# Optimization experiments

Hardware: AMD Instinct MI355X
Metric: run time of the kernel (lower is better)

The kernel has to match this reference:

```python
import jax, jax.numpy as jnp
import numpy as np
from jax import lax

B, N, C, RED = 8, 2048, 1024, 4
GN_EPS = 1e-5


def setup_inputs() -> dict:
    key = jax.random.key(0)
    ks = jax.random.split(key, 8)
    s = lambda k, shp, sc: jax.random.normal(k, shp, jnp.float32) * sc
    return dict(
        x=jax.random.normal(ks[0], (B, N, C), jnp.float32),
        qkv_w=s(ks[1], (C, 3 * C), 0.02),
        c1=jnp.float32(0.01 ** 2),
        c2=jnp.float32(0.03 ** 2),
        conv1_w=s(ks[2], (4, 1, 3), 0.3),      # OIH
        gn_g=jnp.ones(4, jnp.float32),
        gn_b=jnp.zeros(4, jnp.float32),
        conv2_w=s(ks[3], (1, 4, 3), 0.3),      # OIH
        conv2_b=jnp.zeros(1, jnp.float32),
        ch_w1=s(ks[4], (C, C // RED), 0.02),
        ch_b1=jnp.zeros(C // RED, jnp.float32),
        ch_w2=s(ks[5], (C // RED, C), 0.02),
        ch_b2=jnp.zeros(C, jnp.float32),
        proj_w=s(ks[6], (C, C), 0.02),
        proj_b=jnp.zeros(C, jnp.float32),
    )


def _conv1d(x, w):  # x:[B,Cin,N], w:[O,I,3], pad=1
    return lax.conv_general_dilated(x, w, (1,), [(1, 1)],
                                    dimension_numbers=('NCH', 'OIH', 'NCH'))


def _ode_func(A, conv1_w, gn_g, gn_b, conv2_w, conv2_b):
    # A: [B,N] -> Conv1d(1,4) -> GroupNorm(2,4) -> ReLU -> Conv1d(4,1)
    h = _conv1d(A[:, None, :], conv1_w)                 # [B,4,N]
    b, _, n = h.shape
    hg = h.reshape(b, 2, 2, n)                          # 2 groups of 2 channels
    mu = hg.mean((2, 3), keepdims=True)
    var = hg.var((2, 3), keepdims=True)
    h = ((hg - mu) * lax.rsqrt(var + GN_EPS)).reshape(b, 4, n)
    h = jax.nn.relu(h * gn_g[None, :, None] + gn_b[None, :, None])
    y = _conv1d(h, conv2_w) + conv2_b[None, :, None]    # [B,1,N]
    return y[:, 0, :]


def reference(x, qkv_w, c1, c2, conv1_w, gn_g, gn_b, conv2_w, conv2_b,
              ch_w1, ch_b1, ch_w2, ch_b2, proj_w, proj_b):
    Bx, Nx, Cx = x.shape
    qkv = (x @ qkv_w).reshape(Bx, Nx, 3, Cx)
    q, k, v = qkv[..., 0, :], qkv[..., 1, :], qkv[..., 2, :]

    # SSIM-style per-token statistics over the channel dim
    mu_q = q.mean(-1, keepdims=True)
    mu_k = k.mean(-1, keepdims=True)
    dq, dk = q - mu_q, k - mu_k
    inv_cm1 = 1.0 / (Cx - 1)
    sigma_qk = (dq * dk).sum(-1, keepdims=True) * inv_cm1
    sigma_q2 = (dq * dq).sum(-1, keepdims=True) * inv_cm1
    sigma_k2 = (dk * dk).sum(-1, keepdims=True) * inv_cm1
    num = (2 * mu_q * mu_k + c1) * (2 * sigma_qk + c2)
    den = (mu_q ** 2 + mu_k ** 2 + c1) * (sigma_q2 + sigma_k2 + c2)
    attn_base = ((num / (den + 1e-7)) ** 2)[..., 0]     # [B,N]

    # explicit-Euler integration over t = linspace(0,1,2) -> one step, dt=1
    steps = 2
    ts = jnp.linspace(0.0, 1.0, steps)
    dts = ts[1:] - ts[:-1]

    def step(A, dt):
        return A + dt * _ode_func(A, conv1_w, gn_g, gn_b, conv2_w, conv2_b), None

    A, _ = lax.scan(step, attn_base, dts)
    final_a = jax.nn.sigmoid(A)                         # [B,N]
    weights = jax.nn.softmax(final_a, axis=1)           # softmax over tokens

    # channel gating from mean token
    m = x.mean(axis=1, keepdims=True)                   # [B,1,C]
    ch_w = jax.nn.sigmoid(jax.nn.relu(m @ ch_w1 + ch_b1) @ ch_w2 + ch_b2)

    out_low = weights[..., None] * v * ch_w             # [B,N,C]
    return out_low @ proj_w + proj_b
```

## Files before the change

kernel.cpp:

```cpp
#include <hip/hip_runtime.h>

typedef __attribute__((ext_vector_type(8))) short short8;
typedef __attribute__((ext_vector_type(4))) short short4v;
typedef __attribute__((ext_vector_type(4))) float floatx4;

__device__ __forceinline__ unsigned short f2bf(float f) {
    unsigned u = __float_as_uint(f);
    u = u + 0x7fffu + ((u >> 16) & 1u);
    return (unsigned short)(u >> 16);
}
__device__ __forceinline__ float bf2f(short s) {
    return __uint_as_float(((unsigned)(unsigned short)s) << 16);
}

__device__ __forceinline__ void gl_lds16(const void* g, void* l) {
    __builtin_amdgcn_global_load_lds((const __attribute__((address_space(1))) void*)g,
                                     (__attribute__((address_space(3))) void*)l, 16, 0, 0);
}

__global__ __launch_bounds__(256) void convmean_kernel(const float* __restrict__ x,
                                                       short* __restrict__ xb,
                                                       float* __restrict__ part) {
    int bid = blockIdx.x;
    int b = bid >> 6, nch = bid & 63;
    int tid = threadIdx.x;
    size_t base = ((size_t)b * 2048 + nch * 32) * 1024;
    float s0 = 0.f, s1 = 0.f, s2 = 0.f, s3 = 0.f;
    int c0 = tid * 4;
    for (int r = 0; r < 32; r++) {
        const float* rp = x + base + (size_t)r * 1024 + c0;
        float4 v = *(const float4*)rp;
        s0 += v.x; s1 += v.y; s2 += v.z; s3 += v.w;
        short4v o;
        o[0] = (short)f2bf(v.x); o[1] = (short)f2bf(v.y);
        o[2] = (short)f2bf(v.z); o[3] = (short)f2bf(v.w);
        *(short4v*)(xb + base + (size_t)r * 1024 + c0) = o;
    }
    float* pp = part + ((size_t)b * 64 + nch) * 1024 + c0;
    float4 ps; ps.x = s0; ps.y = s1; ps.z = s2; ps.w = s3;
    *(float4*)pp = ps;
}

__global__ __launch_bounds__(256) void transpose_conv_kernel(const float* __restrict__ w_qkv,
                                                             short* __restrict__ qkvT,
                                                             const float* __restrict__ w_proj,
                                                             short* __restrict__ projT) {
    __shared__ float t[64][65];
    int bx = blockIdx.x;
    const float* in; short* out; int C; bool is_qkv;
    int c0, r0 = blockIdx.y * 64;
    if (bx < 48) { in = w_qkv; out = qkvT; C = 3072; c0 = bx * 64; is_qkv = true; }
    else         { in = w_proj; out = projT; C = 1024; c0 = (bx - 48) * 64; is_qkv = false; }
    int tid = threadIdx.x;
#pragma unroll
    for (int l = 0; l < 16; l++) {
        int idx = l * 256 + tid;
        int rr = idx >> 6, cc = idx & 63;
        t[rr][cc] = in[(size_t)(r0 + rr) * C + c0 + cc];
    }
    __syncthreads();
#pragma unroll
    for (int l = 0; l < 16; l++) {
        int idx = l * 256 + tid;
        int rr = idx >> 6, cc = idx & 63;
        int ro = c0 + rr;
        int rnew = ro;
        if (is_qkv) {
            if (ro < 1024) rnew = 2 * ro;
            else if (ro < 2048) rnew = 2 * (ro - 1024) + 1;
        }
        out[(size_t)rnew * 1024 + r0 + cc] = (short)f2bf(t[cc][rr]);
    }
}

__global__ __launch_bounds__(256) void ch_kernel(const float* __restrict__ part,
                                                 const float* __restrict__ w1,
                                                 const float* __restrict__ b1,
                                                 const float* __restrict__ w2,
                                                 const float* __restrict__ b2,
                                                 float* __restrict__ ch) {
    int b = blockIdx.x >> 3, cg = blockIdx.x & 7;
    int tid = threadIdx.x;
    __shared__ float mrow[1024];
    __shared__ float hid[256];
    for (int i = tid; i < 1024; i += 256) {
        float s = 0.f;
        for (int j = 0; j < 64; j++) s += part[((size_t)b * 64 + j) * 1024 + i];
        mrow[i] = s * (1.f / 2048.f);
    }
    __syncthreads();
    {
        float s0 = 0.f, s1 = 0.f, s2 = 0.f, s3 = 0.f;
        for (int i = 0; i < 1024; i += 4) {
            s0 += mrow[i] * w1[(size_t)i * 256 + tid];
            s1 += mrow[i + 1] * w1[(size_t)(i + 1) * 256 + tid];
            s2 += mrow[i + 2] * w1[(size_t)(i + 2) * 256 + tid];
            s3 += mrow[i + 3] * w1[(size_t)(i + 3) * 256 + tid];
        }
        hid[tid] = fmaxf((s0 + s1) + (s2 + s3) + b1[tid], 0.f);
    }
    __syncthreads();
    if (tid < 128) {
        int c = cg * 128 + tid;
        float s0 = 0.f, s1 = 0.f, s2 = 0.f, s3 = 0.f;
        for (int j = 0; j < 256; j += 4) {
            s0 += hid[j] * w2[(size_t)j * 1024 + c];
            s1 += hid[j + 1] * w2[(size_t)(j + 1) * 1024 + c];
            s2 += hid[j + 2] * w2[(size_t)(j + 2) * 1024 + c];
            s3 += hid[j + 3] * w2[(size_t)(j + 3) * 1024 + c];
        }
        float s = (s0 + s1) + (s2 + s3) + b2[c];
        ch[(size_t)b * 1024 + c] = 1.f / (1.f + expf(-s));
    }
}

__global__ __launch_bounds__(256, 4) void gemm_qkv_kernel(const short* __restrict__ A,
                                                          const short* __restrict__ BT,
                                                          short* __restrict__ vbuf,
                                                          const float* __restrict__ ch,
                                                          float* __restrict__ part2)
{
    __shared__ __align__(16) short Ash[2 * 128 * 32];
    __shared__ __align__(16) short Bsh[2 * 128 * 32];
    const int tid = threadIdx.x;
    const int wave = tid >> 6, lane = tid & 63;
    const int id = blockIdx.x;
    const int xcd = id & 7, j = id >> 3;
    const int half = j / 192;
    const int rem = j % 192;
    const int bmi = rem & 7;
    const int bn = rem >> 3;
    const int bm = (half * 8 + bmi) * 8 + xcd;
    const int wm = wave >> 1, wn = wave & 1;
    const int l4 = lane >> 2, kk = (lane & 3) * 8;
    const int lda = 1024, ldb = 1024;

    const short* Ag = A + (size_t)(bm * 128 + wave * 32 + l4) * lda + kk;
    const short* Bg = BT + (size_t)(bn * 128 + wave * 32 + l4) * ldb + kk;
    short* lA = Ash + wave * 1024;
    short* lB = Bsh + wave * 1024;

    floatx4 acc[4][4];
    floatx4 zero = {0.f, 0.f, 0.f, 0.f};
#pragma unroll
    for (int i = 0; i < 4; i++)
#pragma unroll
        for (int jj = 0; jj < 4; jj++) acc[i][jj] = zero;

    const int ar = lane & 15, ak = (lane >> 4) * 8;
    const int quad = lane >> 4;

    for (int k0 = 0; k0 < 1024; k0 += 64) {
#pragma unroll
        for (int h = 0; h < 2; h++) {
            gl_lds16(Ag + k0 + h * 32, lA + h * 4096);
            gl_lds16(Ag + 16 * lda + k0 + h * 32, lA + h * 4096 + 512);
            gl_lds16(Bg + k0 + h * 32, lB + h * 4096);
            gl_lds16(Bg + 16 * ldb + k0 + h * 32, lB + h * 4096 + 512);
        }
        __syncthreads();
#pragma unroll
        for (int h = 0; h < 2; h++) {
            short8 af[4], bfr[4];
#pragma unroll
            for (int t = 0; t < 4; t++)
                af[t] = *(const short8*)(Ash + h * 4096 + (wm * 64 + t * 16 + ar) * 32 + ak);
#pragma unroll
            for (int t = 0; t < 4; t++)
                bfr[t] = *(const short8*)(Bsh + h * 4096 + (wn * 64 + t * 16 + ar) * 32 + ak);
#pragma unroll
            for (int i = 0; i < 4; i++)
#pragma unroll
                for (int jj = 0; jj < 4; jj++)
                    acc[i][jj] = __builtin_amdgcn_mfma_f32_16x16x32_bf16(af[i], bfr[jj], acc[i][jj], 0, 0, 0);
        }
        __syncthreads();
    }

    if (bn < 16) {
        float* sb = (float*)Ash;
#pragma unroll
        for (int i = 0; i < 4; i++) {
            float st[4][5];
#pragma unroll
            for (int r = 0; r < 4; r++)
#pragma unroll
                for (int f = 0; f < 5; f++) st[r][f] = 0.f;
#pragma unroll
            for (int jj = 0; jj < 4; jj++) {
#pragma unroll
                for (int r = 0; r < 4; r++) {
                    float val = acc[i][jj][r];
                    float other = __shfl_xor(val, 1);
                    float q = (lane & 1) ? other : val;
                    float kv = (lane & 1) ? val : other;
                    st[r][0] += q; st[r][1] += kv;
                    st[r][2] += q * q; st[r][3] += kv * kv; st[r][4] += q * kv;
                }
            }
#pragma unroll
            for (int r = 0; r < 4; r++)
#pragma unroll
                for (int f = 0; f < 5; f++) {
                    float v = st[r][f];
                    v += __shfl_xor(v, 2);
                    v += __shfl_xor(v, 4);
                    v += __shfl_xor(v, 8);
                    st[r][f] = v;
                }
            if ((lane & 15) == 0) {
#pragma unroll
                for (int r = 0; r < 4; r++)
#pragma unroll
                    for (int f = 0; f < 5; f++)
                        sb[(size_t)(wn * 128 + wm * 64 + i * 16 + quad * 4 + r) * 5 + f] = st[r][f];
            }
        }
        __syncthreads();
        if (tid < 128) {
            int grow = bm * 128 + tid;
#pragma unroll
            for (int f = 0; f < 5; f++) {
                float s = sb[(size_t)tid * 5 + f] + sb[(size_t)(128 + tid) * 5 + f];
                part2[(size_t)(bn * 5 + f) * 16384 + grow] = s;
            }
        }
    } else {
        const int batch = (bm * 128) >> 11;
        const int vcol0 = bn * 128 - 2048 + wn * 64;
        short* pbuf = Ash + wave * 1024;
        float cw[4];
#pragma unroll
        for (int jj = 0; jj < 4; jj++) cw[jj] = ch[(size_t)batch * 1024 + vcol0 + jj * 16 + ar];
#pragma unroll
        for (int i = 0; i < 4; i++) {
#pragma unroll
            for (int jj = 0; jj < 4; jj++)
#pragma unroll
                for (int r = 0; r < 4; r++)
                    pbuf[(quad * 4 + r) * 64 + jj * 16 + ar] = (short)f2bf(acc[i][jj][r] * cw[jj]);
#pragma unroll
            for (int p = 0; p < 2; p++) {
                int idx = p * 512 + lane * 8;
                short8 vv = *(const short8*)(pbuf + idx);
                int grow = bm * 128 + wm * 64 + i * 16 + (idx >> 6);
                int gcol = vcol0 + (idx & 63);
                *(short8*)(vbuf + (size_t)grow * 1024 + gcol) = vv;
            }
        }
    }
}

__global__ __launch_bounds__(256) void finalize_kernel(const float* __restrict__ part2,
                                                       const float* __restrict__ c1p,
                                                       const float* __restrict__ c2p,
                                                       float* __restrict__ attn) {
    int row = blockIdx.x * 256 + threadIdx.x;
    float s[5] = {0.f, 0.f, 0.f, 0.f, 0.f};
#pragma unroll
    for (int slot = 0; slot < 16; slot++)
#pragma unroll
        for (int f = 0; f < 5; f++)
            s[f] += part2[(size_t)((slot * 5 + f) << 14) + row];
    const float C = 1024.f, invcm1 = 1.f / 1023.f;
    float c1 = *c1p, c2 = *c2p;
    float muq = s[0] / C, muk = s[1] / C;
    float sigqk = (s[4] - C * muq * muk) * invcm1;
    float sigq2 = (s[2] - C * muq * muq) * invcm1;
    float sigk2 = (s[3] - C * muk * muk) * invcm1;
    float num = (2.f * muq * muk + c1) * (2.f * sigqk + c2);
    float den = (muq * muq + muk * muk + c1) * (sigq2 + sigk2 + c2);
    float r = num / (den + 1e-7f);
    attn[row] = r * r;
}

__device__ __forceinline__ float blk_sum(float v, float* buf) {
#pragma unroll
    for (int m = 1; m < 64; m <<= 1) v += __shfl_xor(v, m);
    int wave = threadIdx.x >> 6;
    if ((threadIdx.x & 63) == 0) buf[wave] = v;
    __syncthreads();
    float r = buf[0] + buf[1] + buf[2] + buf[3];
    __syncthreads();
    return r;
}
__device__ __forceinline__ float blk_max(float v, float* buf) {
#pragma unroll
    for (int m = 1; m < 64; m <<= 1) v = fmaxf(v, __shfl_xor(v, m));
    int wave = threadIdx.x >> 6;
    if ((threadIdx.x & 63) == 0) buf[wave] = v;
    __syncthreads();
    float r = fmaxf(fmaxf(buf[0], buf[1]), fmaxf(buf[2], buf[3]));
    __syncthreads();
    return r;
}

__global__ __launch_bounds__(256) void ode_softmax_kernel(const float* __restrict__ attn,
                                                          const float* __restrict__ w1,
                                                          const float* __restrict__ gng,
                                                          const float* __restrict__ gnb,
                                                          const float* __restrict__ w2,
                                                          const float* __restrict__ b2,
                                                          float* __restrict__ wgt) {
    int b = blockIdx.x, tid = threadIdx.x;
    __shared__ float A0[2048];
    __shared__ float H[4][2048];
    __shared__ float rbuf[4];
    for (int i = tid; i < 2048; i += 256) A0[i] = attn[(size_t)b * 2048 + i];
    __syncthreads();
    float w1l[12], w2l[12];
#pragma unroll
    for (int i = 0; i < 12; i++) { w1l[i] = w1[i]; w2l[i] = w2[i]; }
    float gg[4], gb[4];
#pragma unroll
    for (int c = 0; c < 4; c++) { gg[c] = gng[c]; gb[c] = gnb[c]; }

    float s0 = 0.f, ss0 = 0.f, s1 = 0.f, ss1 = 0.f;
    for (int i = tid; i < 2048; i += 256) {
        float le = (i > 0) ? A0[i - 1] : 0.f;
        float mi = A0[i];
        float ri = (i < 2047) ? A0[i + 1] : 0.f;
#pragma unroll
        for (int c = 0; c < 4; c++) {
            float h = w1l[c * 3] * le + w1l[c * 3 + 1] * mi + w1l[c * 3 + 2] * ri;
            H[c][i] = h;
            if (c < 2) { s0 += h; ss0 += h * h; } else { s1 += h; ss1 += h * h; }
        }
    }
    s0 = blk_sum(s0, rbuf);
    ss0 = blk_sum(ss0, rbuf);
    s1 = blk_sum(s1, rbuf);
    ss1 = blk_sum(ss1, rbuf);
    float mu0 = s0 / 4096.f, var0 = ss0 / 4096.f - mu0 * mu0;
    float mu1 = s1 / 4096.f, var1 = ss1 / 4096.f - mu1 * mu1;
    float is0 = 1.f / sqrtf(var0 + 1e-5f);
    float is1 = 1.f / sqrtf(var1 + 1e-5f);

    for (int i = tid; i < 2048; i += 256) {
#pragma unroll
        for (int c = 0; c < 4; c++) {
            float inv = (c < 2) ? is0 : is1;
            float mu = (c < 2) ? mu0 : mu1;
            float v = (H[c][i] - mu) * inv * gg[c] + gb[c];
            H[c][i] = fmaxf(v, 0.f);
        }
    }
    __syncthreads();

    float bias2 = b2[0];
    float myfa[8];
    float lmax = -1e30f;
#pragma unroll
    for (int ii = 0; ii < 8; ii++) {
        int i = tid + ii * 256;
        float y = bias2;
#pragma unroll
        for (int c = 0; c < 4; c++) {
            float le = (i > 0) ? H[c][i - 1] : 0.f;
            float mi = H[c][i];
            float ri = (i < 2047) ? H[c][i + 1] : 0.f;
            y += w2l[c * 3] * le + w2l[c * 3 + 1] * mi + w2l[c * 3 + 2] * ri;
        }
        float Av = A0[i] + y;
        float fa = 1.f / (1.f + expf(-Av));
        myfa[ii] = fa;
        lmax = fmaxf(lmax, fa);
    }
    float gmax = blk_max(lmax, rbuf);
    float lsum = 0.f;
#pragma unroll
    for (int ii = 0; ii < 8; ii++) {
        myfa[ii] = expf(myfa[ii] - gmax);
        lsum += myfa[ii];
    }
    float gsum = blk_sum(lsum, rbuf);
    float inv = 1.f / gsum;
#pragma unroll
    for (int ii = 0; ii < 8; ii++) wgt[(size_t)b * 2048 + tid + ii * 256] = myfa[ii] * inv;
}

__global__ __launch_bounds__(256, 4) void gemm_out_kernel(const short* __restrict__ vbuf,
                                                          const short* __restrict__ BT,
                                                          const float* __restrict__ wgt,
                                                          const float* __restrict__ pb,
                                                          float* __restrict__ Out)
{
    __shared__ __align__(16) short Ash[2 * 128 * 32];
    __shared__ __align__(16) short Bsh[2 * 128 * 32];
    const int tid = threadIdx.x;
    const int wave = tid >> 6, lane = tid & 63;
    const int id = blockIdx.x;
    const int xcd = id & 7, j = id >> 3;
    const int half = j >> 6;
    const int rem = j & 63;
    const int bmi = rem & 7;
    const int bn = rem >> 3;
    const int bm = (half * 8 + bmi) * 8 + xcd;
    const int wm = wave >> 1, wn = wave & 1;
    const int l4 = lane >> 2, kk = (lane & 3) * 8;
    const int lda = 1024, ldb = 1024;

    const short* Ag = vbuf + (size_t)(bm * 128 + wave * 32 + l4) * lda + kk;
    const short* Bg = BT + (size_t)(bn * 128 + wave * 32 + l4) * ldb + kk;
    short* lA = Ash + wave * 1024;
    short* lB = Bsh + wave * 1024;

    floatx4 acc[4][4];
    floatx4 zero = {0.f, 0.f, 0.f, 0.f};
#pragma unroll
    for (int i = 0; i < 4; i++)
#pragma unroll
        for (int jj = 0; jj < 4; jj++) acc[i][jj] = zero;

    const int ar = lane & 15, ak = (lane >> 4) * 8;
    const int quad = lane >> 4;

    for (int k0 = 0; k0 < 1024; k0 += 64) {
#pragma unroll
        for (int h = 0; h < 2; h++) {
            gl_lds16(Ag + k0 + h * 32, lA + h * 4096);
            gl_lds16(Ag + 16 * lda + k0 + h * 32, lA + h * 4096 + 512);
            gl_lds16(Bg + k0 + h * 32, lB + h * 4096);
            gl_lds16(Bg + 16 * ldb + k0 + h * 32, lB + h * 4096 + 512);
        }
        __syncthreads();
#pragma unroll
        for (int h = 0; h < 2; h++) {
            short8 af[4], bfr[4];
#pragma unroll
            for (int t = 0; t < 4; t++)
                af[t] = *(const short8*)(Ash + h * 4096 + (wm * 64 + t * 16 + ar) * 32 + ak);
#pragma unroll
            for (int t = 0; t < 4; t++)
                bfr[t] = *(const short8*)(Bsh + h * 4096 + (wn * 64 + t * 16 + ar) * 32 + ak);
#pragma unroll
            for (int i = 0; i < 4; i++)
#pragma unroll
                for (int jj = 0; jj < 4; jj++)
                    acc[i][jj] = __builtin_amdgcn_mfma_f32_16x16x32_bf16(af[i], bfr[jj], acc[i][jj], 0, 0, 0);
        }
        __syncthreads();
    }

    const int row0 = bm * 128 + wm * 64;
    const int col0 = bn * 128 + wn * 64;
    float* obuf = (float*)Ash + wave * 1024;
#pragma unroll
    for (int i = 0; i < 4; i++) {
#pragma unroll
        for (int jj = 0; jj < 4; jj++) {
            float bias = pb[col0 + jj * 16 + ar];
#pragma unroll
            for (int r = 0; r < 4; r++) {
                int grow = row0 + i * 16 + quad * 4 + r;
                obuf[(quad * 4 + r) * 64 + jj * 16 + ar] = wgt[grow] * acc[i][jj][r] + bias;
            }
        }
#pragma unroll
        for (int p = 0; p < 4; p++) {
            int idx = p * 256 + lane * 4;
            float4 vv = *(const float4*)(obuf + idx);
            int grow = row0 + i * 16 + (idx >> 6);
            int gcol = col0 + (idx & 63);
            *(float4*)(Out + (size_t)grow * 1024 + gcol) = vv;
        }
    }
}

extern "C" void kernel_launch(void* const* d_in, const int* in_sizes, int n_in,
                              void* d_out, int out_size, void* d_ws, size_t ws_size,
                              hipStream_t stream) {
    const float* x       = (const float*)d_in[0];
    const float* qkv_w   = (const float*)d_in[1];
    const float* c1      = (const float*)d_in[2];
    const float* c2      = (const float*)d_in[3];
    const float* conv1_w = (const float*)d_in[4];
    const float* gn_g    = (const float*)d_in[5];
    const float* gn_b    = (const float*)d_in[6];
    const float* conv2_w = (const float*)d_in[7];
    const float* conv2_b = (const float*)d_in[8];
    const float* ch_w1   = (const float*)d_in[9];
    const float* ch_b1   = (const float*)d_in[10];
    const float* ch_w2   = (const float*)d_in[11];
    const float* ch_b2   = (const float*)d_in[12];
    const float* proj_w  = (const float*)d_in[13];
    const float* proj_b  = (const float*)d_in[14];
    float* out = (float*)d_out;

    size_t off = 0;
    char* base = (char*)d_ws;
    auto carve = [&](size_t bytes) -> char* {
        char* p = base + off;
        off += (bytes + 255) & ~(size_t)255;
        return p;
    };
    short* x_bf  = (short*)carve((size_t)16384 * 1024 * 2);
    short* qkvT  = (short*)carve((size_t)3072 * 1024 * 2);
    short* projT = (short*)carve((size_t)1024 * 1024 * 2);
    short* vbuf  = (short*)carve((size_t)16384 * 1024 * 2);
    float* part2 = (float*)carve((size_t)80 * 16384 * 4);
    float* attn  = (float*)carve((size_t)16384 * 4);
    float* wgt   = (float*)carve((size_t)16384 * 4);
    float* part  = (float*)carve((size_t)8 * 64 * 1024 * 4);
    float* chw   = (float*)carve((size_t)8 * 1024 * 4);

    convmean_kernel<<<512, 256, 0, stream>>>(x, x_bf, part);
    transpose_conv_kernel<<<dim3(64, 16), 256, 0, stream>>>(qkv_w, qkvT, proj_w, projT);
    ch_kernel<<<64, 256, 0, stream>>>(part, ch_w1, ch_b1, ch_w2, ch_b2, chw);
    gemm_qkv_kernel<<<3072, 256, 0, stream>>>(x_bf, qkvT, vbuf, chw, part2);
    finalize_kernel<<<64, 256, 0, stream>>>(part2, c1, c2, attn);
    ode_softmax_kernel<<<8, 256, 0, stream>>>(attn, conv1_w, gn_g, gn_b, conv2_w, conv2_b, wgt);
    gemm_out_kernel<<<1024, 256, 0, stream>>>(vbuf, projT, wgt, proj_b, out);
}
```

Before: 394.2 us.

## Pipeline GEMM main loops with 4-stage LDS ring, XOR swizzle, single barrier

Both bf16 GEMM kernels (QKV and output projection) now use a 4-slot LDS ring buffer with 3 stages of global-to-LDS prefetch in flight. Each K-step of 32 needs only one barrier, gated by explicit vmcnt waits, in place of the old synchronous load/sync/compute/sync loop over K=64. The staging addresses and fragment reads are XOR-swizzled to avoid LDS bank conflicts, and MFMA sections are wrapped in s_setprio. LDS use doubles and launch bounds drop to 2 blocks per CU, trading occupancy for latency hiding.

```diff
diff --git a/kernel.cpp b/kernel.cpp
--- a/kernel.cpp
+++ b/kernel.cpp
@@ -114,14 +114,14 @@
     }
 }
 
-__global__ __launch_bounds__(256, 4) void gemm_qkv_kernel(const short* __restrict__ A,
+__global__ __launch_bounds__(256, 2) void gemm_qkv_kernel(const short* __restrict__ A,
                                                           const short* __restrict__ BT,
                                                           short* __restrict__ vbuf,
                                                           const float* __restrict__ ch,
                                                           float* __restrict__ part2)
 {
-    __shared__ __align__(16) short Ash[2 * 128 * 32];
-    __shared__ __align__(16) short Bsh[2 * 128 * 32];
+    __shared__ __align__(16) short AS[4][4096];
+    __shared__ __align__(16) short BS[4][4096];
     const int tid = threadIdx.x;
     const int wave = tid >> 6, lane = tid & 63;
     const int id = blockIdx.x;
@@ -132,13 +132,11 @@
     const int bn = rem >> 3;
     const int bm = (half * 8 + bmi) * 8 + xcd;
     const int wm = wave >> 1, wn = wave & 1;
-    const int l4 = lane >> 2, kk = (lane & 3) * 8;
-    const int lda = 1024, ldb = 1024;
-
-    const short* Ag = A + (size_t)(bm * 128 + wave * 32 + l4) * lda + kk;
-    const short* Bg = BT + (size_t)(bn * 128 + wave * 32 + l4) * ldb + kk;
-    short* lA = Ash + wave * 1024;
-    short* lB = Bsh + wave * 1024;
+
+    const int swzk = (((lane & 3) ^ ((lane >> 3) & 3)) << 3);
+    const int stoff = wave * 1024 + lane * 8;
+    const short* Ag = A + (size_t)(bm * 128 + wave * 32 + (lane >> 2)) * 1024 + swzk;
+    const short* Bg = BT + (size_t)(bn * 128 + wave * 32 + (lane >> 2)) * 1024 + swzk;
 
     floatx4 acc[4][4];
     floatx4 zero = {0.f, 0.f, 0.f, 0.f};
@@ -147,38 +145,66 @@
 #pragma unroll
         for (int jj = 0; jj < 4; jj++) acc[i][jj] = zero;
 
-    const int ar = lane & 15, ak = (lane >> 4) * 8;
+    const int ar = lane & 15;
     const int quad = lane >> 4;
-
-    for (int k0 = 0; k0 < 1024; k0 += 64) {
-#pragma unroll
-        for (int h = 0; h < 2; h++) {
-            gl_lds16(Ag + k0 + h * 32, lA + h * 4096);
-            gl_lds16(Ag + 16 * lda + k0 + h * 32, lA + h * 4096 + 512);
-            gl_lds16(Bg + k0 + h * 32, lB + h * 4096);
-            gl_lds16(Bg + 16 * ldb + k0 + h * 32, lB + h * 4096 + 512);
-        }
-        __syncthreads();
-#pragma unroll
-        for (int h = 0; h < 2; h++) {
-            short8 af[4], bfr[4];
-#pragma unroll
-            for (int t = 0; t < 4; t++)
-                af[t] = *(const short8*)(Ash + h * 4096 + (wm * 64 + t * 16 + ar) * 32 + ak);
-#pragma unroll
-            for (int t = 0; t < 4; t++)
-                bfr[t] = *(const short8*)(Bsh + h * 4096 + (wn * 64 + t * 16 + ar) * 32 + ak);
-#pragma unroll
-            for (int i = 0; i < 4; i++)
-#pragma unroll
-                for (int jj = 0; jj < 4; jj++)
-                    acc[i][jj] = __builtin_amdgcn_mfma_f32_16x16x32_bf16(af[i], bfr[jj], acc[i][jj], 0, 0, 0);
-        }
-        __syncthreads();
-    }
+    const int sr8 = ((lane >> 4) ^ ((lane >> 1) & 3)) << 3;
+
+    auto stage = [&](int t) {
+        const int sl = t & 3, ko = t * 32;
+        gl_lds16(Ag + ko,          AS[sl] + stoff);
+        gl_lds16(Ag + 16384 + ko,  AS[sl] + stoff + 512);
+        gl_lds16(Bg + ko,          BS[sl] + stoff);
+        gl_lds16(Bg + 16384 + ko,  BS[sl] + stoff + 512);
+    };
+    auto compute = [&](int t) {
+        const short* As_ = AS[t & 3];
+        const short* Bs_ = BS[t & 3];
+        short8 af[4], bfr[4];
+#pragma unroll
+        for (int q = 0; q < 4; q++)
+            af[q] = *(const short8*)(As_ + (wm * 64 + q * 16 + ar) * 32 + sr8);
+#pragma unroll
+        for (int q = 0; q < 4; q++)
+            bfr[q] = *(const short8*)(Bs_ + (wn * 64 + q * 16 + ar) * 32 + sr8);
+        __builtin_amdgcn_s_setprio(1);
+#pragma unroll
+        for (int i = 0; i < 4; i++)
+#pragma unroll
+            for (int jj = 0; jj < 4; jj++)
+                acc[i][jj] = __builtin_amdgcn_mfma_f32_16x16x32_bf16(af[i], bfr[jj], acc[i][jj], 0, 0, 0);
+        __builtin_amdgcn_s_setprio(0);
+    };
+
+    stage(0); stage(1); stage(2);
+#pragma unroll 4
+    for (int t = 0; t < 28; ++t) {
+        asm volatile("s_waitcnt vmcnt(8) lgkmcnt(0)" ::: "memory");
+        __builtin_amdgcn_s_barrier();
+        asm volatile("" ::: "memory");
+        stage(t + 3);
+        compute(t);
+    }
+    asm volatile("s_waitcnt vmcnt(8) lgkmcnt(0)" ::: "memory");
+    __builtin_amdgcn_s_barrier();
+    asm volatile("" ::: "memory");
+    stage(31);
+    compute(28);
+    asm volatile("s_waitcnt vmcnt(8) lgkmcnt(0)" ::: "memory");
+    __builtin_amdgcn_s_barrier();
+    asm volatile("" ::: "memory");
+    compute(29);
+    asm volatile("s_waitcnt vmcnt(4) lgkmcnt(0)" ::: "memory");
+    __builtin_amdgcn_s_barrier();
+    asm volatile("" ::: "memory");
+    compute(30);
+    asm volatile("s_waitcnt vmcnt(0) lgkmcnt(0)" ::: "memory");
+    __builtin_amdgcn_s_barrier();
+    asm volatile("" ::: "memory");
+    compute(31);
+    __syncthreads();
 
     if (bn < 16) {
-        float* sb = (float*)Ash;
+        float* sb = (float*)AS;
 #pragma unroll
         for (int i = 0; i < 4; i++) {
             float st[4][5];
@@ -228,7 +254,7 @@
     } else {
         const int batch = (bm * 128) >> 11;
         const int vcol0 = bn * 128 - 2048 + wn * 64;
-        short* pbuf = Ash + wave * 1024;
+        short* pbuf = (short*)AS + wave * 1024;
         float cw[4];
 #pragma unroll
         for (int jj = 0; jj < 4; jj++) cw[jj] = ch[(size_t)batch * 1024 + vcol0 + jj * 16 + ar];
@@ -379,14 +405,14 @@
     for (int ii = 0; ii < 8; ii++) wgt[(size_t)b * 2048 + tid + ii * 256] = myfa[ii] * inv;
 }
 
-__global__ __launch_bounds__(256, 4) void gemm_out_kernel(const short* __restrict__ vbuf,
+__global__ __launch_bounds__(256, 2) void gemm_out_kernel(const short* __restrict__ vbuf,
                                                           const short* __restrict__ BT,
                                                           const float* __restrict__ wgt,
                                                           const float* __restrict__ pb,
                                                           float* __restrict__ Out)
 {
-    __shared__ __align__(16) short Ash[2 * 128 * 32];
-    __shared__ __align__(16) short Bsh[2 * 128 * 32];
+    __shared__ __align__(16) short AS[4][4096];
+    __shared__ __align__(16) short BS[4][4096];
     const int tid = threadIdx.x;
     const int wave = tid >> 6, lane = tid & 63;
     const int id = blockIdx.x;
@@ -397,13 +423,11 @@
     const int bn = rem >> 3;
     const int bm = (half * 8 + bmi) * 8 + xcd;
     const int wm = wave >> 1, wn = wave & 1;
-    const int l4 = lane >> 2, kk = (lane & 3) * 8;
-    const int lda = 1024, ldb = 1024;
-
-    const short* Ag = vbuf + (size_t)(bm * 128 + wave * 32 + l4) * lda + kk;
-    const short* Bg = BT + (size_t)(bn * 128 + wave * 32 + l4) * ldb + kk;
-    short* lA = Ash + wave * 1024;
-    short* lB = Bsh + wave * 1024;
+
+    const int swzk = (((lane & 3) ^ ((lane >> 3) & 3)) << 3);
+    const int stoff = wave * 1024 + lane * 8;
+    const short* Ag = vbuf + (size_t)(bm * 128 + wave * 32 + (lane >> 2)) * 1024 + swzk;
+    const short* Bg = BT + (size_t)(bn * 128 + wave * 32 + (lane >> 2)) * 1024 + swzk;
 
     floatx4 acc[4][4];
     floatx4 zero = {0.f, 0.f, 0.f, 0.f};
@@ -412,39 +436,67 @@
 #pragma unroll
         for (int jj = 0; jj < 4; jj++) acc[i][jj] = zero;
 
-    const int ar = lane & 15, ak = (lane >> 4) * 8;
+    const int ar = lane & 15;
     const int quad = lane >> 4;
-
-    for (int k0 = 0; k0 < 1024; k0 += 64) {
-#pragma unroll
-        for (int h = 0; h < 2; h++) {
-            gl_lds16(Ag + k0 + h * 32, lA + h * 4096);
-            gl_lds16(Ag + 16 * lda + k0 + h * 32, lA + h * 4096 + 512);
-            gl_lds16(Bg + k0 + h * 32, lB + h * 4096);
-            gl_lds16(Bg + 16 * ldb + k0 + h * 32, lB + h * 4096 + 512);
-        }
-        __syncthreads();
-#pragma unroll
-        for (int h = 0; h < 2; h++) {
-            short8 af[4], bfr[4];
-#pragma unroll
-            for (int t = 0; t < 4; t++)
-                af[t] = *(const short8*)(Ash + h * 4096 + (wm * 64 + t * 16 + ar) * 32 + ak);
-#pragma unroll
-            for (int t = 0; t < 4; t++)
-                bfr[t] = *(const short8*)(Bsh + h * 4096 + (wn * 64 + t * 16 + ar) * 32 + ak);
-#pragma unroll
-            for (int i = 0; i < 4; i++)
-#pragma unroll
-                for (int jj = 0; jj < 4; jj++)
-                    acc[i][jj] = __builtin_amdgcn_mfma_f32_16x16x32_bf16(af[i], bfr[jj], acc[i][jj], 0, 0, 0);
-        }
-        __syncthreads();
-    }
+    const int sr8 = ((lane >> 4) ^ ((lane >> 1) & 3)) << 3;
+
+    auto stage = [&](int t) {
+        const int sl = t & 3, ko = t * 32;
+        gl_lds16(Ag + ko,          AS[sl] + stoff);
+        gl_lds16(Ag + 16384 + ko,  AS[sl] + stoff + 512);
+        gl_lds16(Bg + ko,          BS[sl] + stoff);
+        gl_lds16(Bg + 16384 + ko,  BS[sl] + stoff + 512);
+    };
+    auto compute = [&](int t) {
+        const short* As_ = AS[t & 3];
+        const short* Bs_ = BS[t & 3];
+        short8 af[4], bfr[4];
+#pragma unroll
+        for (int q = 0; q < 4; q++)
+            af[q] = *(const short8*)(As_ + (wm * 64 + q * 16 + ar) * 32 + sr8);
+#pragma unroll
+        for (int q = 0; q < 4; q++)
+            bfr[q] = *(const short8*)(Bs_ + (wn * 64 + q * 16 + ar) * 32 + sr8);
+        __builtin_amdgcn_s_setprio(1);
+#pragma unroll
+        for (int i = 0; i < 4; i++)
+#pragma unroll
+            for (int jj = 0; jj < 4; jj++)
+                acc[i][jj] = __builtin_amdgcn_mfma_f32_16x16x32_bf16(af[i], bfr[jj], acc[i][jj], 0, 0, 0);
+        __builtin_amdgcn_s_setprio(0);
+    };
+
+    stage(0); stage(1); stage(2);
+#pragma unroll 4
+    for (int t = 0; t < 28; ++t) {
+        asm volatile("s_waitcnt vmcnt(8) lgkmcnt(0)" ::: "memory");
+        __builtin_amdgcn_s_barrier();
+        asm volatile("" ::: "memory");
+        stage(t + 3);
+        compute(t);
+    }
+    asm volatile("s_waitcnt vmcnt(8) lgkmcnt(0)" ::: "memory");
+    __builtin_amdgcn_s_barrier();
+    asm volatile("" ::: "memory");
+    stage(31);
+    compute(28);
+    asm volatile("s_waitcnt vmcnt(8) lgkmcnt(0)" ::: "memory");
+    __builtin_amdgcn_s_barrier();
+    asm volatile("" ::: "memory");
+    compute(29);
+    asm volatile("s_waitcnt vmcnt(4) lgkmcnt(0)" ::: "memory");
+    __builtin_amdgcn_s_barrier();
+    asm volatile("" ::: "memory");
+    compute(30);
+    asm volatile("s_waitcnt vmcnt(0) lgkmcnt(0)" ::: "memory");
+    __builtin_amdgcn_s_barrier();
+    asm volatile("" ::: "memory");
+    compute(31);
+    __syncthreads();
 
     const int row0 = bm * 128 + wm * 64;
     const int col0 = bn * 128 + wn * 64;
-    float* obuf = (float*)Ash + wave * 1024;
+    float* obuf = (float*)AS + wave * 1024;
 #pragma unroll
     for (int i = 0; i < 4; i++) {
 #pragma unroll
```

Result: slower. 420.9 us (+6.8%).

## Use 256x256 tiles with 4-stage async LDS pipeline in both GEMMs

Applied to the files above, without the earlier changes.

Both bf16 GEMMs move from 128x128 tiles with 4 waves and a load-then-sync loop to 256x256 tiles with 8 waves. A 4-slot ring of K=32 slices is filled by global_load_lds, with manual vmcnt waits and split barriers so loads overlap the MFMA work, and s_setprio raises priority around the MFMA bursts. The larger tile halves the partial-stat slots the finalize kernel reads, and it raises arithmetic intensity. In exchange it uses more LDS and registers per block and launches fewer blocks (768 and 256), which could hurt occupancy and tail balance on the GPU.

```diff
diff --git a/kernel.cpp b/kernel.cpp
--- a/kernel.cpp
+++ b/kernel.cpp
@@ -8,9 +8,6 @@
     unsigned u = __float_as_uint(f);
     u = u + 0x7fffu + ((u >> 16) & 1u);
     return (unsigned short)(u >> 16);
-}
-__device__ __forceinline__ float bf2f(short s) {
-    return __uint_as_float(((unsigned)(unsigned short)s) << 16);
 }
 
 __device__ __forceinline__ void gl_lds16(const void* g, void* l) {
@@ -114,73 +111,111 @@
     }
 }
 
-__global__ __launch_bounds__(256, 4) void gemm_qkv_kernel(const short* __restrict__ A,
+
+#define QKV_PHASE(qq)                                                                   \
+    {                                                                                   \
+        _Pragma("unroll")                                                               \
+        for (int ii = 0; ii < 4; ii++)                                                  \
+            af[ii] = *(const short8*)(As_ + (wm * 128 + ((qq)*4 + ii) * 16 + ar) * 32 + quad * 8); \
+        __builtin_amdgcn_s_setprio(1);                                                  \
+        _Pragma("unroll")                                                               \
+        for (int ii = 0; ii < 4; ii++)                                                  \
+            _Pragma("unroll")                                                           \
+            for (int jj = 0; jj < 4; jj++)                                              \
+                acc[(qq)*4 + ii][jj] =                                                  \
+                    __builtin_amdgcn_mfma_f32_16x16x32_bf16(af[ii], bfr[jj], acc[(qq)*4 + ii][jj], 0, 0, 0); \
+        __builtin_amdgcn_s_setprio(0);                                                  \
+    }
+
+#define LOAD_B()                                                                        \
+    {                                                                                   \
+        _Pragma("unroll")                                                               \
+        for (int jj = 0; jj < 4; jj++)                                                  \
+            bfr[jj] = *(const short8*)(Bs_ + (wn * 64 + jj * 16 + ar) * 32 + quad * 8); \
+    }
+
+__global__ __launch_bounds__(512, 2) void gemm_qkv_kernel(const short* __restrict__ A,
                                                           const short* __restrict__ BT,
                                                           short* __restrict__ vbuf,
                                                           const float* __restrict__ ch,
                                                           float* __restrict__ part2)
 {
-    __shared__ __align__(16) short Ash[2 * 128 * 32];
-    __shared__ __align__(16) short Bsh[2 * 128 * 32];
+    __shared__ __align__(16) short ASf[4 * 8192];
+    __shared__ __align__(16) short BSf[4 * 8192];
     const int tid = threadIdx.x;
     const int wave = tid >> 6, lane = tid & 63;
     const int id = blockIdx.x;
     const int xcd = id & 7, j = id >> 3;
-    const int half = j / 192;
-    const int rem = j % 192;
-    const int bmi = rem & 7;
-    const int bn = rem >> 3;
-    const int bm = (half * 8 + bmi) * 8 + xcd;
-    const int wm = wave >> 1, wn = wave & 1;
-    const int l4 = lane >> 2, kk = (lane & 3) * 8;
-    const int lda = 1024, ldb = 1024;
-
-    const short* Ag = A + (size_t)(bm * 128 + wave * 32 + l4) * lda + kk;
-    const short* Bg = BT + (size_t)(bn * 128 + wave * 32 + l4) * ldb + kk;
-    short* lA = Ash + wave * 1024;
-    short* lB = Bsh + wave * 1024;
-
-    floatx4 acc[4][4];
+    const int bn = j % 12;
+    const int bmg = j / 12;
+    const int bm = bmg * 8 + xcd;
+    const int wm = wave >> 2, wn = wave & 3;
+    const int ar = lane & 15, quad = lane >> 4;
+
+    const short* Ag = A + (size_t)(bm * 256 + wave * 32 + (lane >> 2)) * 1024 + (lane & 3) * 8;
+    const short* Bg = BT + (size_t)(bn * 256 + wave * 32 + (lane >> 2)) * 1024 + (lane & 3) * 8;
+    short* ASw = ASf + wave * 1024;
+    short* BSw = BSf + wave * 1024;
+
+    floatx4 acc[8][4];
     floatx4 zero = {0.f, 0.f, 0.f, 0.f};
 #pragma unroll
-    for (int i = 0; i < 4; i++)
+    for (int i = 0; i < 8; i++)
 #pragma unroll
         for (int jj = 0; jj < 4; jj++) acc[i][jj] = zero;
 
-    const int ar = lane & 15, ak = (lane >> 4) * 8;
-    const int quad = lane >> 4;
-
-    for (int k0 = 0; k0 < 1024; k0 += 64) {
-#pragma unroll
-        for (int h = 0; h < 2; h++) {
-            gl_lds16(Ag + k0 + h * 32, lA + h * 4096);
-            gl_lds16(Ag + 16 * lda + k0 + h * 32, lA + h * 4096 + 512);
-            gl_lds16(Bg + k0 + h * 32, lB + h * 4096);
-            gl_lds16(Bg + 16 * ldb + k0 + h * 32, lB + h * 4096 + 512);
-        }
-        __syncthreads();
-#pragma unroll
-        for (int h = 0; h < 2; h++) {
-            short8 af[4], bfr[4];
-#pragma unroll
-            for (int t = 0; t < 4; t++)
-                af[t] = *(const short8*)(Ash + h * 4096 + (wm * 64 + t * 16 + ar) * 32 + ak);
-#pragma unroll
-            for (int t = 0; t < 4; t++)
-                bfr[t] = *(const short8*)(Bsh + h * 4096 + (wn * 64 + t * 16 + ar) * 32 + ak);
-#pragma unroll
-            for (int i = 0; i < 4; i++)
-#pragma unroll
-                for (int jj = 0; jj < 4; jj++)
-                    acc[i][jj] = __builtin_amdgcn_mfma_f32_16x16x32_bf16(af[i], bfr[jj], acc[i][jj], 0, 0, 0);
-        }
-        __syncthreads();
-    }
-
-    if (bn < 16) {
-        float* sb = (float*)Ash;
-#pragma unroll
-        for (int i = 0; i < 4; i++) {
+    auto stageA = [&](int t) {
+        const int sl = (t & 3) * 8192, ko = t * 32;
+        gl_lds16(Ag + ko, ASw + sl);
+        gl_lds16(Ag + (size_t)16 * 1024 + ko, ASw + sl + 512);
+    };
+    auto stageB = [&](int t) {
+        const int sl = (t & 3) * 8192, ko = t * 32;
+        gl_lds16(Bg + ko, BSw + sl);
+        gl_lds16(Bg + (size_t)16 * 1024 + ko, BSw + sl + 512);
+    };
+
+    short8 af[4], bfr[4];
+
+    stageA(0); stageB(0); stageA(1); stageB(1);
+    for (int t = 0; t < 30; ++t) {
+        stageA(t + 2);
+        asm volatile("s_waitcnt vmcnt(6)" ::: "memory");
+        asm volatile("s_barrier" ::: "memory");
+        const short* As_ = ASf + (t & 3) * 8192;
+        const short* Bs_ = BSf + (t & 3) * 8192;
+        LOAD_B();
+        QKV_PHASE(0);
+        stageB(t + 2);
+        asm volatile("s_barrier" ::: "memory");
+        QKV_PHASE(1);
+    }
+    {
+        asm volatile("s_waitcnt vmcnt(4)" ::: "memory");
+        asm volatile("s_barrier" ::: "memory");
+        const short* As_ = ASf + (30 & 3) * 8192;
+        const short* Bs_ = BSf + (30 & 3) * 8192;
+        LOAD_B();
+        QKV_PHASE(0);
+        asm volatile("s_barrier" ::: "memory");
+        QKV_PHASE(1);
+    }
+    {
+        asm volatile("s_waitcnt vmcnt(0)" ::: "memory");
+        asm volatile("s_barrier" ::: "memory");
+        const short* As_ = ASf + (31 & 3) * 8192;
+        const short* Bs_ = BSf + (31 & 3) * 8192;
+        LOAD_B();
+        QKV_PHASE(0);
+        asm volatile("s_barrier" ::: "memory");
+        QKV_PHASE(1);
+    }
+    __syncthreads();
+
+    if (bn < 8) {
+        float* sb = (float*)ASf;
+#pragma unroll
+        for (int i = 0; i < 8; i++) {
             float st[4][5];
 #pragma unroll
             for (int r = 0; r < 4; r++)
@@ -213,27 +248,27 @@
                 for (int r = 0; r < 4; r++)
 #pragma unroll
                     for (int f = 0; f < 5; f++)
-                        sb[(size_t)(wn * 128 + wm * 64 + i * 16 + quad * 4 + r) * 5 + f] = st[r][f];
+                        sb[(size_t)(wn * 256 + wm * 128 + i * 16 + quad * 4 + r) * 5 + f] = st[r][f];
             }
         }
         __syncthreads();
-        if (tid < 128) {
-            int grow = bm * 128 + tid;
+        if (tid < 256) {
 #pragma unroll
             for (int f = 0; f < 5; f++) {
-                float s = sb[(size_t)tid * 5 + f] + sb[(size_t)(128 + tid) * 5 + f];
-                part2[(size_t)(bn * 5 + f) * 16384 + grow] = s;
+                float s = sb[(size_t)(0 * 256 + tid) * 5 + f] + sb[(size_t)(1 * 256 + tid) * 5 + f] +
+                          sb[(size_t)(2 * 256 + tid) * 5 + f] + sb[(size_t)(3 * 256 + tid) * 5 + f];
+                part2[(size_t)(bn * 5 + f) * 16384 + bm * 256 + tid] = s;
             }
         }
     } else {
-        const int batch = (bm * 128) >> 11;
-        const int vcol0 = bn * 128 - 2048 + wn * 64;
-        short* pbuf = Ash + wave * 1024;
+        const int batch = bm >> 3;
+        const int vcol0 = bn * 256 - 2048 + wn * 64;
+        short* pbuf = (short*)ASf + wave * 1024;
         float cw[4];
 #pragma unroll
         for (int jj = 0; jj < 4; jj++) cw[jj] = ch[(size_t)batch * 1024 + vcol0 + jj * 16 + ar];
 #pragma unroll
-        for (int i = 0; i < 4; i++) {
+        for (int i = 0; i < 8; i++) {
 #pragma unroll
             for (int jj = 0; jj < 4; jj++)
 #pragma unroll
@@ -243,7 +278,7 @@
             for (int p = 0; p < 2; p++) {
                 int idx = p * 512 + lane * 8;
                 short8 vv = *(const short8*)(pbuf + idx);
-                int grow = bm * 128 + wm * 64 + i * 16 + (idx >> 6);
+                int grow = bm * 256 + wm * 128 + i * 16 + (idx >> 6);
                 int gcol = vcol0 + (idx & 63);
                 *(short8*)(vbuf + (size_t)grow * 1024 + gcol) = vv;
             }
@@ -258,7 +293,7 @@
     int row = blockIdx.x * 256 + threadIdx.x;
     float s[5] = {0.f, 0.f, 0.f, 0.f, 0.f};
 #pragma unroll
-    for (int slot = 0; slot < 16; slot++)
+    for (int slot = 0; slot < 8; slot++)
 #pragma unroll
         for (int f = 0; f < 5; f++)
             s[f] += part2[(size_t)((slot * 5 + f) << 14) + row];
@@ -379,74 +414,89 @@
     for (int ii = 0; ii < 8; ii++) wgt[(size_t)b * 2048 + tid + ii * 256] = myfa[ii] * inv;
 }
 
-__global__ __launch_bounds__(256, 4) void gemm_out_kernel(const short* __restrict__ vbuf,
+__global__ __launch_bounds__(512, 2) void gemm_out_kernel(const short* __restrict__ vbuf,
                                                           const short* __restrict__ BT,
                                                           const float* __restrict__ wgt,
                                                           const float* __restrict__ pb,
                                                           float* __restrict__ Out)
 {
-    __shared__ __align__(16) short Ash[2 * 128 * 32];
-    __shared__ __align__(16) short Bsh[2 * 128 * 32];
+    __shared__ __align__(16) short ASf[4 * 8192];
+    __shared__ __align__(16) short BSf[4 * 8192];
     const int tid = threadIdx.x;
     const int wave = tid >> 6, lane = tid & 63;
     const int id = blockIdx.x;
     const int xcd = id & 7, j = id >> 3;
-    const int half = j >> 6;
-    const int rem = j & 63;
-    const int bmi = rem & 7;
-    const int bn = rem >> 3;
-    const int bm = (half * 8 + bmi) * 8 + xcd;
-    const int wm = wave >> 1, wn = wave & 1;
-    const int l4 = lane >> 2, kk = (lane & 3) * 8;
-    const int lda = 1024, ldb = 1024;
-
-    const short* Ag = vbuf + (size_t)(bm * 128 + wave * 32 + l4) * lda + kk;
-    const short* Bg = BT + (size_t)(bn * 128 + wave * 32 + l4) * ldb + kk;
-    short* lA = Ash + wave * 1024;
-    short* lB = Bsh + wave * 1024;
-
-    floatx4 acc[4][4];
+    const int bn = j & 3;
+    const int bmg = j >> 2;
+    const int bm = bmg * 8 + xcd;
+    const int wm = wave >> 2, wn = wave & 3;
+    const int ar = lane & 15, quad = lane >> 4;
+
+    const short* Ag = vbuf + (size_t)(bm * 256 + wave * 32 + (lane >> 2)) * 1024 + (lane & 3) * 8;
+    const short* Bg = BT + (size_t)(bn * 256 + wave * 32 + (lane >> 2)) * 1024 + (lane & 3) * 8;
+    short* ASw = ASf + wave * 1024;
+    short* BSw = BSf + wave * 1024;
+
+    floatx4 acc[8][4];
     floatx4 zero = {0.f, 0.f, 0.f, 0.f};
 #pragma unroll
-    for (int i = 0; i < 4; i++)
+    for (int i = 0; i < 8; i++)
 #pragma unroll
         for (int jj = 0; jj < 4; jj++) acc[i][jj] = zero;
 
-    const int ar = lane & 15, ak = (lane >> 4) * 8;
-    const int quad = lane >> 4;
-
-    for (int k0 = 0; k0 < 1024; k0 += 64) {
-#pragma unroll
-        for (int h = 0; h < 2; h++) {
-            gl_lds16(Ag + k0 + h * 32, lA + h * 4096);
-            gl_lds16(Ag + 16 * lda + k0 + h * 32, lA + h * 4096 + 512);
-            gl_lds16(Bg + k0 + h * 32, lB + h * 4096);
-            gl_lds16(Bg + 16 * ldb + k0 + h * 32, lB + h * 4096 + 512);
-        }
-        __syncthreads();
-#pragma unroll
-        for (int h = 0; h < 2; h++) {
-            short8 af[4], bfr[4];
-#pragma unroll
-            for (int t = 0; t < 4; t++)
-                af[t] = *(const short8*)(Ash + h * 4096 + (wm * 64 + t * 16 + ar) * 32 + ak);
-#pragma unroll
-            for (int t = 0; t < 4; t++)
-                bfr[t] = *(const short8*)(Bsh + h * 4096 + (wn * 64 + t * 16 + ar) * 32 + ak);
-#pragma unroll
-            for (int i = 0; i < 4; i++)
-#pragma unroll
-                for (int jj = 0; jj < 4; jj++)
-                    acc[i][jj] = __builtin_amdgcn_mfma_f32_16x16x32_bf16(af[i], bfr[jj], acc[i][jj], 0, 0, 0);
-        }
-        __syncthreads();
-    }
-
-    const int row0 = bm * 128 + wm * 64;
-    const int col0 = bn * 128 + wn * 64;
-    float* obuf = (float*)Ash + wave * 1024;
-#pragma unroll
-    for (int i = 0; i < 4; i++) {
+    auto stageA = [&](int t) {
+        const int sl = (t & 3) * 8192, ko = t * 32;
+        gl_lds16(Ag + ko, ASw + sl);
+        gl_lds16(Ag + (size_t)16 * 1024 + ko, ASw + sl + 512);
+    };
+    auto stageB = [&](int t) {
+        const int sl = (t & 3) * 8192, ko = t * 32;
+        gl_lds16(Bg + ko, BSw + sl);
+        gl_lds16(Bg + (size_t)16 * 1024 + ko, BSw + sl + 512);
+    };
+
+    short8 af[4], bfr[4];
+
+    stageA(0); stageB(0); stageA(1); stageB(1);
+    for (int t = 0; t < 30; ++t) {
+        stageA(t + 2);
+        asm volatile("s_waitcnt vmcnt(6)" ::: "memory");
+        asm volatile("s_barrier" ::: "memory");
+        const short* As_ = ASf + (t & 3) * 8192;
+        const short* Bs_ = BSf + (t & 3) * 8192;
+        LOAD_B();
+        QKV_PHASE(0);
+        stageB(t + 2);
+        asm volatile("s_barrier" ::: "memory");
+        QKV_PHASE(1);
+    }
+    {
+        asm volatile("s_waitcnt vmcnt(4)" ::: "memory");
+        asm volatile("s_barrier" ::: "memory");
+        const short* As_ = ASf + (30 & 3) * 8192;
+        const short* Bs_ = BSf + (30 & 3) * 8192;
+        LOAD_B();
+        QKV_PHASE(0);
+        asm volatile("s_barrier" ::: "memory");
+        QKV_PHASE(1);
+    }
+    {
+        asm volatile("s_waitcnt vmcnt(0)" ::: "memory");
+        asm volatile("s_barrier" ::: "memory");
+        const short* As_ = ASf + (31 & 3) * 8192;
+        const short* Bs_ = BSf + (31 & 3) * 8192;
+        LOAD_B();
+        QKV_PHASE(0);
+        asm volatile("s_barrier" ::: "memory");
+        QKV_PHASE(1);
+    }
+    __syncthreads();
+
+    const int row0 = bm * 256 + wm * 128;
+    const int col0 = bn * 256 + wn * 64;
+    float* obuf = (float*)ASf + wave * 1024;
+#pragma unroll
+    for (int i = 0; i < 8; i++) {
 #pragma unroll
         for (int jj = 0; jj < 4; jj++) {
             float bias = pb[col0 + jj * 16 + ar];
@@ -507,8 +557,8 @@
     convmean_kernel<<<512, 256, 0, stream>>>(x, x_bf, part);
     transpose_conv_kernel<<<dim3(64, 16), 256, 0, stream>>>(qkv_w, qkvT, proj_w, projT);
     ch_kernel<<<64, 256, 0, stream>>>(part, ch_w1, ch_b1, ch_w2, ch_b2, chw);
-    gemm_qkv_kernel<<<3072, 256, 0, stream>>>(x_bf, qkvT, vbuf, chw, part2);
+    gemm_qkv_kernel<<<768, 512, 0, stream>>>(x_bf, qkvT, vbuf, chw, part2);
     finalize_kernel<<<64, 256, 0, stream>>>(part2, c1, c2, attn);
     ode_softmax_kernel<<<8, 256, 0, stream>>>(attn, conv1_w, gn_g, gn_b, conv2_w, conv2_b, wgt);
-    gemm_out_kernel<<<1024, 256, 0, stream>>>(vbuf, projT, wgt, proj_b, out);
-}
+    gemm_out_kernel<<<256, 512, 0, stream>>>(vbuf, projT, wgt, proj_b, out);
+}
```

Result: no change. 398.8 us (+1.1%).
